# Kernel tuning notes

Measured on AMD Instinct MI355X. Metric: run time of the kernel, lower is better.

Reference implementation:

```python
import jax, jax.numpy as jnp
import numpy as np


def _build_idx():
    # Gather indices replicating the 36 overlapping 3x3 window slices.
    # Board layout: flat index = x*48 + y*6 + f  (8x8 squares, 6 features).
    idx = np.zeros((36, 54), dtype=np.int32)
    for i in range(36):
        x, y = i // 6, i % 6
        c = 0
        for ox in range(3):
            for oy in range(3):
                base = (x + ox) * 48 + (y + oy) * 6
                for f in range(6):
                    idx[i, c] = base + f
                    c += 1
    return jnp.asarray(idx)

IDX = _build_idx()  # [36, 54]
B = 65536


def setup_inputs() -> dict:
    key = jax.random.key(0)
    ks = jax.random.split(key, 13)
    rn = lambda k, shape, s=0.3: jax.random.normal(k, shape, dtype=jnp.float32) * s
    return {
        "inp": jax.random.normal(ks[0], (B, 385), dtype=jnp.float32),
        "W1": rn(ks[1], (16, 54)), "b1": rn(ks[2], (16,)),
        "W2": rn(ks[3], (16, 16)), "b2": rn(ks[4], (16,)),
        "W3": rn(ks[5], (2, 16)),  "b3": rn(ks[6], (2,)),
        "E1": rn(ks[7], (34, 73)), "e1": rn(ks[8], (34,)),
        "E2": rn(ks[9], (34, 34)), "e2": rn(ks[10], (34,)),
        "E3": rn(ks[11], (1, 34)), "e3": rn(ks[12], (1,)),
    }


def reference(inp, W1, b1, W2, b2, W3, b3, E1, e1, E2, e2, E3, e3):
    crelu = lambda x: jnp.clip(x, -1.0, 1.0)
    # One gather replaces 36 * 9 slice/cat ops: [B, 36, 54]
    w = inp[:, IDX]
    # Sight MLP applied to all 36 windows at once (torch Linear: x @ W.T + b)
    h = crelu(jnp.einsum('bws,os->bwo', w, W1) + b1)   # [B, 36, 16]
    h = crelu(jnp.einsum('bwi,oi->bwo', h, W2) + b2)   # [B, 36, 16]
    v = crelu(jnp.einsum('bwi,oi->bwo', h, W3) + b3)   # [B, 36, 2]
    # vision[i*2], vision[i*2+1] interleave == reshape of [36, 2]; append inp[384]
    vision = jnp.concatenate([v.reshape(v.shape[0], 72), inp[:, 384:385]], axis=-1)  # [B, 73]
    h = crelu(vision @ E1.T + e1)
    h = crelu(h @ E2.T + e2)
    return crelu(h @ E3.T + e3)  # [B, 1]
```

## Files before the change

### kernel.cpp

```cpp
#include <hip/hip_runtime.h>
#include <hip/hip_fp16.h>

typedef _Float16 half8v __attribute__((ext_vector_type(8)));
typedef __fp16  pk16x2 __attribute__((ext_vector_type(2)));
typedef float f32x4 __attribute__((ext_vector_type(4)));

#define DEV __device__ __forceinline__
DEV float crelu(float x) { return fminf(fmaxf(x, -1.0f), 1.0f); }

DEV unsigned int pkrtz_u32(float a, float b) {
    pk16x2 p = __builtin_amdgcn_cvt_pkrtz(a, b);
    return __builtin_bit_cast(unsigned int, p);
}

DEV void lgkm0() { asm volatile("s_waitcnt lgkmcnt(0)" ::: "memory"); }
DEV void cfence() { asm volatile("" ::: "memory"); }

__global__ void prep_kernel(const float* __restrict__ W1, const float* __restrict__ W2,
                            const float* __restrict__ W3, const float* __restrict__ E1,
                            const float* __restrict__ E2, const float* __restrict__ e1b,
                            const float* __restrict__ e2b, const float* __restrict__ E3,
                            float* __restrict__ ws) {
    int t = threadIdx.x + blockIdx.x * blockDim.x;
    if (t < 864) {
        int s = t >> 4, o = t & 15;
        ws[t] = W1[o * 54 + s];
    } else if (t < 864 + 256) {
        int u = t - 864; int i = u >> 4, o = u & 15;
        ws[t] = W2[o * 16 + i];
    } else if (t < 1120 + 32) {
        int u = t - 1120; int i = u >> 1, o = u & 1;
        ws[t] = W3[o * 16 + i];
    } else if (t >= 8192 && t < 8192 + 1536) {
        _Float16* fr = (_Float16*)((char*)ws + 19200);
        int u = t - 8192;
        int ks = u >> 9, l = (u >> 3) & 63, j = u & 7;
        int n = l & 15;
        int kg = ks * 32 + ((l >> 4) << 3) + j;
        int ox = kg / 24, rem = kg - ox * 24, cy = rem >> 3, f = rem & 7;
        float v = (kg < 72 && f < 6) ? W1[n * 54 + ox * 18 + cy * 6 + f] : 0.0f;
        fr[u] = (_Float16)v;
    } else if (t >= 10240 && t < 10240 + 512) {
        _Float16* fr = (_Float16*)((char*)ws + 19200) + 1536;
        int u = t - 10240;
        int l = u >> 3, j = u & 7;
        int n = l & 15;
        int k = ((l >> 4) << 3) + j;
        float v = (k < 16) ? W2[n * 16 + k] : 0.0f;
        fr[u] = (_Float16)v;
    } else if (t >= 12288 && t < 12288 + 4608) {
        _Float16* fr = (_Float16*)((char*)ws + 32768);
        int u = t - 12288;
        int ks = u / 1536, rem = u % 1536;
        int nt = rem / 512;
        int l = (rem >> 3) & 63, j = u & 7;
        int k = ks * 32 + ((l >> 4) << 3) + j;
        int o = nt * 16 + (l & 15);
        float v = (k < 73 && o < 34) ? E1[o * 73 + k] : 0.0f;
        fr[u] = (_Float16)v;
    } else if (t >= 18432 && t < 18432 + 3072) {
        _Float16* fr = (_Float16*)((char*)ws + 45056);
        int u = t - 18432;
        int ks = u / 1536, rem = u % 1536;
        int nt = rem / 512;
        int l = (rem >> 3) & 63, j = u & 7;
        int k = ks * 32 + ((l >> 4) << 3) + j;
        int o = nt * 16 + (l & 15);
        float v = (k < 34 && o < 34) ? E2[o * 34 + k] : 0.0f;
        fr[u] = (_Float16)v;
    } else if (t >= 22528 && t < 22528 + 48) {
        int u = t - 22528; ws[6000 + u] = (u < 34) ? e1b[u] : 0.0f;
    } else if (t >= 22592 && t < 22592 + 48) {
        int u = t - 22592; ws[6048 + u] = (u < 34) ? e2b[u] : 0.0f;
    } else if (t >= 22656 && t < 22656 + 48) {
        int u = t - 22656; ws[6096 + u] = (u < 34) ? E3[u] : 0.0f;
    }
}

__global__ __launch_bounds__(256, 3) void win_kernel(
    const float* __restrict__ inp,
    const float* __restrict__ b1, const float* __restrict__ b2,
    const float* __restrict__ b3,
    const float* __restrict__ ws, const _Float16* __restrict__ frag,
    unsigned int* __restrict__ vout)
{
    __shared__ half8v lds[4 * 580];
    const int tid  = threadIdx.x;
    const int wid  = tid >> 6;
    const int lane = tid & 63;
    const int baseP = (blockIdx.x * 4 + wid) * 4;

    half8v* grid = lds + wid * 580;
    half8v* h1   = grid + 288;
    _Float16* h1h = (_Float16*)h1;

    const int r = lane & 15;
    const int g = lane >> 4;

    {
        const uint4 z = {0u, 0u, 0u, 0u};
        #pragma unroll
        for (int i = 0; i < 10; ++i) {
            const int idx = lane + i * 64;
            if (i < 9 || idx < 580)
                *reinterpret_cast<uint4*>(grid + idx) = z;
        }
    }
    cfence();

    {
        const int es = lane >> 4, m = lane & 15;
        const float* __restrict__ src = inp + (size_t)(baseP + es) * 385 + 24 * m;
        #pragma unroll
        for (int c = 0; c < 4; ++c) {
            float f0 = src[c * 6 + 0], f1 = src[c * 6 + 1], f2 = src[c * 6 + 2];
            float f3 = src[c * 6 + 3], f4 = src[c * 6 + 4], f5 = src[c * 6 + 5];
            uint4 q;
            q.x = pkrtz_u32(f0, f1);
            q.y = pkrtz_u32(f2, f3);
            q.z = pkrtz_u32(f4, f5);
            q.w = q.z;
            *reinterpret_cast<uint4*>(grid + es * 72 + 4 * m + c) = q;
        }
    }
    cfence();

    const half8v* __restrict__ fr8 = (const half8v*)frag;
    half8v B1_0 = fr8[0 * 64 + lane];
    half8v B1_1 = fr8[1 * 64 + lane];
    half8v B1_2 = fr8[2 * 64 + lane];
    half8v B2f  = fr8[3 * 64 + lane];

    int off[3];
    #pragma unroll
    for (int ks = 0; ks < 3; ++ks) {
        int c = ks * 4 + g;
        int ox = c / 3, cy = c - 3 * ox;
        off[ks] = ox * 8 + cy;
    }

    const float bias1 = b1[r];
    const float bias2 = b2[r];
    const float* __restrict__ w3t = ws + 1120;
    const float b30 = b3[0], b31 = b3[1];

    int w = r, ebase = 0;
    #pragma unroll
    for (int t = 0; t < 9; ++t) {
        const int x = (w * 43) >> 8;
        const int y = w - x * 6;
        const int cellb = ebase + x * 8 + y;

        half8v a0 = grid[cellb + off[0]];
        half8v a1 = grid[cellb + off[1]];
        half8v a2 = grid[cellb + off[2]];

        f32x4 acc = {bias1, bias1, bias1, bias1};
        acc = __builtin_amdgcn_mfma_f32_16x16x32_f16(a0, B1_0, acc, 0, 0, 0);
        acc = __builtin_amdgcn_mfma_f32_16x16x32_f16(a1, B1_1, acc, 0, 0, 0);
        acc = __builtin_amdgcn_mfma_f32_16x16x32_f16(a2, B1_2, acc, 0, 0, 0);

        #pragma unroll
        for (int q = 0; q < 4; ++q)
            h1h[(t * 16 + g * 4 + q) * 16 + r] = (_Float16)crelu(acc[q]);
        cfence();

        half8v af = h1[(t * 16 + r) * 2 + g];
        f32x4 c2 = {bias2, bias2, bias2, bias2};
        c2 = __builtin_amdgcn_mfma_f32_16x16x32_f16(af, B2f, c2, 0, 0, 0);

        #pragma unroll
        for (int q = 0; q < 4; ++q)
            h1h[(t * 16 + g * 4 + q) * 16 + r] = (_Float16)crelu(c2[q]);

        w += 16;
        if (w >= 36) { w -= 36; ebase += 72; }
    }
    cfence();

    #pragma unroll
    for (int rep = 0; rep < 3; ++rep) {
        const int wg = lane + rep * 64;
        if (rep < 2 || lane < 16) {
            half8v ha = h1[wg * 2 + 0];
            half8v hb = h1[wg * 2 + 1];
            float v0 = b30, v1 = b31;
            #pragma unroll
            for (int i = 0; i < 8; ++i) {
                const float hv = (float)ha[i];
                v0 = fmaf(hv, w3t[i * 2 + 0], v0);
                v1 = fmaf(hv, w3t[i * 2 + 1], v1);
            }
            #pragma unroll
            for (int i = 0; i < 8; ++i) {
                const float hv = (float)hb[i];
                v0 = fmaf(hv, w3t[(8 + i) * 2 + 0], v0);
                v1 = fmaf(hv, w3t[(8 + i) * 2 + 1], v1);
            }
            vout[baseP * 36 + wg] = pkrtz_u32(crelu(v0), crelu(v1));
        }
    }
}

__global__ __launch_bounds__(256) void head3b_kernel(
    const float* __restrict__ inp,
    const float* __restrict__ ws,
    const unsigned int* __restrict__ vbuf,
    const float* __restrict__ e3v,
    float* __restrict__ out)
{
    __shared__ _Float16 hset[4][17 * 48];
    const int tid  = threadIdx.x;
    const int wid  = tid >> 6;
    const int lane = tid & 63;
    const int baseE = (blockIdx.x * 4 + wid) * 16;

    const int r = lane & 15;
    const int g = lane >> 4;
    _Float16* hw = hset[wid];

    {
        const uint4 z = {0u, 0u, 0u, 0u};
        if (lane < 51) {
            *reinterpret_cast<uint4*>(hw + lane * 8) = z;
            *reinterpret_cast<uint4*>(hw + (lane + 51) * 8) = z;
        }
    }
    lgkm0();

    const half8v* __restrict__ e1f8 = (const half8v*)((const char*)ws + 32768);
    const half8v* __restrict__ e2f8 = (const half8v*)((const char*)ws + 45056);

    half8v e1B[3][3], e2B[2][3];
    #pragma unroll
    for (int ks = 0; ks < 3; ++ks)
        #pragma unroll
        for (int nt = 0; nt < 3; ++nt)
            e1B[ks][nt] = e1f8[(ks * 3 + nt) * 64 + lane];
    #pragma unroll
    for (int ks = 0; ks < 2; ++ks)
        #pragma unroll
        for (int nt = 0; nt < 3; ++nt)
            e2B[ks][nt] = e2f8[(ks * 3 + nt) * 64 + lane];

    float biasA[3], bias2A[3], e3w[3];
    #pragma unroll
    for (int nt = 0; nt < 3; ++nt) {
        biasA[nt]  = ws[6000 + nt * 16 + r];
        bias2A[nt] = ws[6048 + nt * 16 + r];
        e3w[nt]    = ws[6096 + nt * 16 + r];
    }

    const uint4* __restrict__ vp4 =
        (const uint4*)(vbuf + (size_t)(baseE + r) * 36);
    const float xl = inp[(size_t)(baseE + r) * 385 + 384];

    f32x4 acc[3] = {{biasA[0], biasA[0], biasA[0], biasA[0]},
                    {biasA[1], biasA[1], biasA[1], biasA[1]},
                    {biasA[2], biasA[2], biasA[2], biasA[2]}};
    #pragma unroll
    for (int ks = 0; ks < 3; ++ks) {
        uint4 aw;
        if (ks < 2) {
            aw = vp4[ks * 4 + g];
        } else {
            if (g == 0)      aw = vp4[8];
            else if (g == 1) { aw.x = pkrtz_u32(xl, 0.0f); aw.y = 0u; aw.z = 0u; aw.w = 0u; }
            else             { aw.x = 0u; aw.y = 0u; aw.z = 0u; aw.w = 0u; }
        }
        const half8v af = __builtin_bit_cast(half8v, aw);
        #pragma unroll
        for (int nt = 0; nt < 3; ++nt)
            acc[nt] = __builtin_amdgcn_mfma_f32_16x16x32_f16(af, e1B[ks][nt],
                                                             acc[nt], 0, 0, 0);
    }

    #pragma unroll
    for (int nt = 0; nt < 3; ++nt)
        #pragma unroll
        for (int q = 0; q < 4; ++q)
            hw[(g * 4 + q) * 48 + nt * 16 + r] = (_Float16)crelu(acc[nt][q]);
    lgkm0();

    f32x4 acc2[3] = {{bias2A[0], bias2A[0], bias2A[0], bias2A[0]},
                     {bias2A[1], bias2A[1], bias2A[1], bias2A[1]},
                     {bias2A[2], bias2A[2], bias2A[2], bias2A[2]}};
    #pragma unroll
    for (int ks = 0; ks < 2; ++ks) {
        const half8v af = *reinterpret_cast<const half8v*>(
            &hw[r * 48 + ks * 32 + g * 8]);
        #pragma unroll
        for (int nt = 0; nt < 3; ++nt)
            acc2[nt] = __builtin_amdgcn_mfma_f32_16x16x32_f16(af, e2B[ks][nt],
                                                              acc2[nt], 0, 0, 0);
    }

    const float e3b = e3v[0];
    float s[4];
    #pragma unroll
    for (int q = 0; q < 4; ++q) {
        float part = crelu(acc2[0][q]) * e3w[0]
                   + crelu(acc2[1][q]) * e3w[1]
                   + crelu(acc2[2][q]) * e3w[2];
        part += __shfl_xor(part, 1);
        part += __shfl_xor(part, 2);
        part += __shfl_xor(part, 4);
        part += __shfl_xor(part, 8);
        s[q] = crelu(part + e3b);
    }
    if (r == 0) {
        float4 o4 = {s[0], s[1], s[2], s[3]};
        *reinterpret_cast<float4*>(out + baseE + g * 4) = o4;
    }
}

extern "C" void kernel_launch(void* const* d_in, const int* in_sizes, int n_in,
                              void* d_out, int out_size, void* d_ws, size_t ws_size,
                              hipStream_t stream) {
    const float* inp = (const float*)d_in[0];
    const float* W1  = (const float*)d_in[1];
    const float* b1  = (const float*)d_in[2];
    const float* W2  = (const float*)d_in[3];
    const float* b2  = (const float*)d_in[4];
    const float* W3  = (const float*)d_in[5];
    const float* b3  = (const float*)d_in[6];
    const float* E1  = (const float*)d_in[7];
    const float* e1  = (const float*)d_in[8];
    const float* E2  = (const float*)d_in[9];
    const float* e2  = (const float*)d_in[10];
    const float* E3  = (const float*)d_in[11];
    const float* e3  = (const float*)d_in[12];
    float* out = (float*)d_out;
    float* ws  = (float*)d_ws;
    const _Float16* frag = (const _Float16*)((const char*)d_ws + 19200);
    unsigned int* vbuf = (unsigned int*)((char*)d_ws + 65536);

    prep_kernel<<<89, 256, 0, stream>>>(W1, W2, W3, E1, E2, e1, e2, E3, ws);

    const int B = 65536;
    win_kernel<<<B / 16, 256, 0, stream>>>(inp, b1, b2, b3, ws, frag, vbuf);
    head3b_kernel<<<B / 64, 256, 0, stream>>>(inp, ws, vbuf, e3, out);
}
```

Baseline: 42.83 us.

## Fuse layer-3 projection into window loop and shrink per-wave LDS buffer

```diff
diff --git a/kernel.cpp b/kernel.cpp
--- a/kernel.cpp
+++ b/kernel.cpp
@@ -2,6 +2,7 @@
 #include <hip/hip_fp16.h>
 
 typedef _Float16 half8v __attribute__((ext_vector_type(8)));
+typedef _Float16 half4v __attribute__((ext_vector_type(4)));
 typedef __fp16  pk16x2 __attribute__((ext_vector_type(2)));
 typedef float f32x4 __attribute__((ext_vector_type(4)));
 
@@ -84,13 +85,13 @@
     const float* __restrict__ ws, const _Float16* __restrict__ frag,
     unsigned int* __restrict__ vout)
 {
-    __shared__ half8v lds[4 * 580];
+    __shared__ half8v lds[4 * 322];
     const int tid  = threadIdx.x;
     const int wid  = tid >> 6;
     const int lane = tid & 63;
     const int baseP = (blockIdx.x * 4 + wid) * 4;
 
-    half8v* grid = lds + wid * 580;
+    half8v* grid = lds + wid * 322;
     half8v* h1   = grid + 288;
     _Float16* h1h = (_Float16*)h1;
 
@@ -100,9 +101,9 @@
     {
         const uint4 z = {0u, 0u, 0u, 0u};
         #pragma unroll
-        for (int i = 0; i < 10; ++i) {
+        for (int i = 0; i < 6; ++i) {
             const int idx = lane + i * 64;
-            if (i < 9 || idx < 580)
+            if (i < 5 || idx < 322)
                 *reinterpret_cast<uint4*>(grid + idx) = z;
         }
     }
@@ -142,6 +143,12 @@
     const float bias1 = b1[r];
     const float bias2 = b2[r];
     const float* __restrict__ w3t = ws + 1120;
+    float w3a[4], w3b[4];
+    #pragma unroll
+    for (int q = 0; q < 4; ++q) {
+        w3a[q] = w3t[(g * 4 + q) * 2 + 0];
+        w3b[q] = w3t[(g * 4 + q) * 2 + 1];
+    }
     const float b30 = b3[0], b31 = b3[1];
 
     int w = r, ebase = 0;
@@ -162,43 +169,42 @@
 
         #pragma unroll
         for (int q = 0; q < 4; ++q)
-            h1h[(t * 16 + g * 4 + q) * 16 + r] = (_Float16)crelu(acc[q]);
+            h1h[(g * 4 + q) * 16 + r] = (_Float16)crelu(acc[q]);
         cfence();
 
-        half8v af = h1[(t * 16 + r) * 2 + g];
+        half8v af = h1[r * 2 + g];
         f32x4 c2 = {bias2, bias2, bias2, bias2};
         c2 = __builtin_amdgcn_mfma_f32_16x16x32_f16(af, B2f, c2, 0, 0, 0);
 
         #pragma unroll
         for (int q = 0; q < 4; ++q)
-            h1h[(t * 16 + g * 4 + q) * 16 + r] = (_Float16)crelu(c2[q]);
+            h1h[(g * 4 + q) * 16 + r] = (_Float16)crelu(c2[q]);
+        cfence();
+
+        {
+            const half4v hq = *reinterpret_cast<const half4v*>(
+                h1h + r * 16 + g * 4);
+            float v0p = 0.0f, v1p = 0.0f;
+            #pragma unroll
+            for (int q = 0; q < 4; ++q) {
+                const float hv = (float)hq[q];
+                v0p = fmaf(hv, w3a[q], v0p);
+                v1p = fmaf(hv, w3b[q], v1p);
+            }
+            v0p += __shfl_xor(v0p, 16);
+            v0p += __shfl_xor(v0p, 32);
+            v1p += __shfl_xor(v1p, 16);
+            v1p += __shfl_xor(v1p, 32);
+            if (g == 0) {
+                const int W = (ebase >> 1) + w;
+                vout[baseP * 36 + W] =
+                    pkrtz_u32(crelu(v0p + b30), crelu(v1p + b31));
+            }
+        }
+        cfence();
 
         w += 16;
         if (w >= 36) { w -= 36; ebase += 72; }
-    }
-    cfence();
-
-    #pragma unroll
-    for (int rep = 0; rep < 3; ++rep) {
-        const int wg = lane + rep * 64;
-        if (rep < 2 || lane < 16) {
-            half8v ha = h1[wg * 2 + 0];
-            half8v hb = h1[wg * 2 + 1];
-            float v0 = b30, v1 = b31;
-            #pragma unroll
-            for (int i = 0; i < 8; ++i) {
-                const float hv = (float)ha[i];
-                v0 = fmaf(hv, w3t[i * 2 + 0], v0);
-                v1 = fmaf(hv, w3t[i * 2 + 1], v1);
-            }
-            #pragma unroll
-            for (int i = 0; i < 8; ++i) {
-                const float hv = (float)hb[i];
-                v0 = fmaf(hv, w3t[(8 + i) * 2 + 0], v0);
-                v1 = fmaf(hv, w3t[(8 + i) * 2 + 1], v1);
-            }
-            vout[baseP * 36 + wg] = pkrtz_u32(crelu(v0), crelu(v1));
-        }
     }
 }
 
```

After: 46.87 us. 1.09x slower.

## Fuse window and head kernels, passing vision through shared memory

Applied to the files above, without the earlier changes.

```diff
diff --git a/kernel.cpp b/kernel.cpp
--- a/kernel.cpp
+++ b/kernel.cpp
@@ -77,22 +77,25 @@
     }
 }
 
-__global__ __launch_bounds__(256, 3) void win_kernel(
+__global__ __launch_bounds__(256, 2) void lila_kernel(
     const float* __restrict__ inp,
     const float* __restrict__ b1, const float* __restrict__ b2,
-    const float* __restrict__ b3,
+    const float* __restrict__ b3, const float* __restrict__ e3v,
     const float* __restrict__ ws, const _Float16* __restrict__ frag,
-    unsigned int* __restrict__ vout)
+    float* __restrict__ out)
 {
     __shared__ half8v lds[4 * 580];
     const int tid  = threadIdx.x;
     const int wid  = tid >> 6;
     const int lane = tid & 63;
-    const int baseP = (blockIdx.x * 4 + wid) * 4;
+    const int baseE = blockIdx.x * 16;
+    const int baseP = baseE + wid * 4;
 
     half8v* grid = lds + wid * 580;
     half8v* h1   = grid + 288;
     _Float16* h1h = (_Float16*)h1;
+    unsigned int* vloc = (unsigned int*)lds;
+    _Float16* hset = (_Float16*)((char*)lds + 9280);
 
     const int r = lane & 15;
     const int g = lane >> 4;
@@ -125,123 +128,101 @@
     }
     cfence();
 
-    const half8v* __restrict__ fr8 = (const half8v*)frag;
-    half8v B1_0 = fr8[0 * 64 + lane];
-    half8v B1_1 = fr8[1 * 64 + lane];
-    half8v B1_2 = fr8[2 * 64 + lane];
-    half8v B2f  = fr8[3 * 64 + lane];
-
-    int off[3];
-    #pragma unroll
-    for (int ks = 0; ks < 3; ++ks) {
-        int c = ks * 4 + g;
-        int ox = c / 3, cy = c - 3 * ox;
-        off[ks] = ox * 8 + cy;
-    }
-
-    const float bias1 = b1[r];
-    const float bias2 = b2[r];
-    const float* __restrict__ w3t = ws + 1120;
-    const float b30 = b3[0], b31 = b3[1];
-
-    int w = r, ebase = 0;
-    #pragma unroll
-    for (int t = 0; t < 9; ++t) {
-        const int x = (w * 43) >> 8;
-        const int y = w - x * 6;
-        const int cellb = ebase + x * 8 + y;
-
-        half8v a0 = grid[cellb + off[0]];
-        half8v a1 = grid[cellb + off[1]];
-        half8v a2 = grid[cellb + off[2]];
-
-        f32x4 acc = {bias1, bias1, bias1, bias1};
-        acc = __builtin_amdgcn_mfma_f32_16x16x32_f16(a0, B1_0, acc, 0, 0, 0);
-        acc = __builtin_amdgcn_mfma_f32_16x16x32_f16(a1, B1_1, acc, 0, 0, 0);
-        acc = __builtin_amdgcn_mfma_f32_16x16x32_f16(a2, B1_2, acc, 0, 0, 0);
-
-        #pragma unroll
-        for (int q = 0; q < 4; ++q)
-            h1h[(t * 16 + g * 4 + q) * 16 + r] = (_Float16)crelu(acc[q]);
-        cfence();
-
-        half8v af = h1[(t * 16 + r) * 2 + g];
-        f32x4 c2 = {bias2, bias2, bias2, bias2};
-        c2 = __builtin_amdgcn_mfma_f32_16x16x32_f16(af, B2f, c2, 0, 0, 0);
-
-        #pragma unroll
-        for (int q = 0; q < 4; ++q)
-            h1h[(t * 16 + g * 4 + q) * 16 + r] = (_Float16)crelu(c2[q]);
-
-        w += 16;
-        if (w >= 36) { w -= 36; ebase += 72; }
-    }
-    cfence();
-
-    #pragma unroll
-    for (int rep = 0; rep < 3; ++rep) {
-        const int wg = lane + rep * 64;
-        if (rep < 2 || lane < 16) {
-            half8v ha = h1[wg * 2 + 0];
-            half8v hb = h1[wg * 2 + 1];
-            float v0 = b30, v1 = b31;
+    {
+        const half8v* __restrict__ fr8 = (const half8v*)frag;
+        half8v B1_0 = fr8[0 * 64 + lane];
+        half8v B1_1 = fr8[1 * 64 + lane];
+        half8v B1_2 = fr8[2 * 64 + lane];
+        half8v B2f  = fr8[3 * 64 + lane];
+
+        int off[3];
+        #pragma unroll
+        for (int ks = 0; ks < 3; ++ks) {
+            int c = ks * 4 + g;
+            int ox = c / 3, cy = c - 3 * ox;
+            off[ks] = ox * 8 + cy;
+        }
+
+        const float bias1 = b1[r];
+        const float bias2 = b2[r];
+
+        int w = r, ebase = 0;
+        #pragma unroll
+        for (int t = 0; t < 9; ++t) {
+            const int x = (w * 43) >> 8;
+            const int y = w - x * 6;
+            const int cellb = ebase + x * 8 + y;
+
+            half8v a0 = grid[cellb + off[0]];
+            half8v a1 = grid[cellb + off[1]];
+            half8v a2 = grid[cellb + off[2]];
+
+            f32x4 acc = {bias1, bias1, bias1, bias1};
+            acc = __builtin_amdgcn_mfma_f32_16x16x32_f16(a0, B1_0, acc, 0, 0, 0);
+            acc = __builtin_amdgcn_mfma_f32_16x16x32_f16(a1, B1_1, acc, 0, 0, 0);
+            acc = __builtin_amdgcn_mfma_f32_16x16x32_f16(a2, B1_2, acc, 0, 0, 0);
+
             #pragma unroll
-            for (int i = 0; i < 8; ++i) {
-                const float hv = (float)ha[i];
-                v0 = fmaf(hv, w3t[i * 2 + 0], v0);
-                v1 = fmaf(hv, w3t[i * 2 + 1], v1);
+            for (int q = 0; q < 4; ++q)
+                h1h[(t * 16 + g * 4 + q) * 16 + r] = (_Float16)crelu(acc[q]);
+            cfence();
+
+            half8v af = h1[(t * 16 + r) * 2 + g];
+            f32x4 c2 = {bias2, bias2, bias2, bias2};
+            c2 = __builtin_amdgcn_mfma_f32_16x16x32_f16(af, B2f, c2, 0, 0, 0);
+
+            #pragma unroll
+            for (int q = 0; q < 4; ++q)
+                h1h[(t * 16 + g * 4 + q) * 16 + r] = (_Float16)crelu(c2[q]);
+
+            w += 16;
+            if (w >= 36) { w -= 36; ebase += 72; }
+        }
+    }
+
+    __syncthreads();
+
+    {
+        const float* __restrict__ w3t = ws + 1120;
+        const float b30 = b3[0], b31 = b3[1];
+        #pragma unroll
+        for (int rep = 0; rep < 3; ++rep) {
+            const int wg = lane + rep * 64;
+            if (rep < 2 || lane < 16) {
+                half8v ha = h1[wg * 2 + 0];
+                half8v hb = h1[wg * 2 + 1];
+                float v0 = b30, v1 = b31;
+                #pragma unroll
+                for (int i = 0; i < 8; ++i) {
+                    const float hv = (float)ha[i];
+                    v0 = fmaf(hv, w3t[i * 2 + 0], v0);
+                    v1 = fmaf(hv, w3t[i * 2 + 1], v1);
+                }
+                #pragma unroll
+                for (int i = 0; i < 8; ++i) {
+                    const float hv = (float)hb[i];
+                    v0 = fmaf(hv, w3t[(8 + i) * 2 + 0], v0);
+                    v1 = fmaf(hv, w3t[(8 + i) * 2 + 1], v1);
+                }
+                vloc[wid * 144 + wg] = pkrtz_u32(crelu(v0), crelu(v1));
             }
-            #pragma unroll
-            for (int i = 0; i < 8; ++i) {
-                const float hv = (float)hb[i];
-                v0 = fmaf(hv, w3t[(8 + i) * 2 + 0], v0);
-                v1 = fmaf(hv, w3t[(8 + i) * 2 + 1], v1);
-            }
-            vout[baseP * 36 + wg] = pkrtz_u32(crelu(v0), crelu(v1));
-        }
-    }
-}
-
-__global__ __launch_bounds__(256) void head3b_kernel(
-    const float* __restrict__ inp,
-    const float* __restrict__ ws,
-    const unsigned int* __restrict__ vbuf,
-    const float* __restrict__ e3v,
-    float* __restrict__ out)
-{
-    __shared__ _Float16 hset[4][17 * 48];
-    const int tid  = threadIdx.x;
-    const int wid  = tid >> 6;
-    const int lane = tid & 63;
-    const int baseE = (blockIdx.x * 4 + wid) * 16;
-
-    const int r = lane & 15;
-    const int g = lane >> 4;
-    _Float16* hw = hset[wid];
+        }
+    }
+
+    __syncthreads();
+    if (wid != 0) return;
 
     {
         const uint4 z = {0u, 0u, 0u, 0u};
         if (lane < 51) {
-            *reinterpret_cast<uint4*>(hw + lane * 8) = z;
-            *reinterpret_cast<uint4*>(hw + (lane + 51) * 8) = z;
+            *reinterpret_cast<uint4*>(hset + lane * 8) = z;
+            *reinterpret_cast<uint4*>(hset + (lane + 51) * 8) = z;
         }
     }
     lgkm0();
 
     const half8v* __restrict__ e1f8 = (const half8v*)((const char*)ws + 32768);
     const half8v* __restrict__ e2f8 = (const half8v*)((const char*)ws + 45056);
-
-    half8v e1B[3][3], e2B[2][3];
-    #pragma unroll
-    for (int ks = 0; ks < 3; ++ks)
-        #pragma unroll
-        for (int nt = 0; nt < 3; ++nt)
-            e1B[ks][nt] = e1f8[(ks * 3 + nt) * 64 + lane];
-    #pragma unroll
-    for (int ks = 0; ks < 2; ++ks)
-        #pragma unroll
-        for (int nt = 0; nt < 3; ++nt)
-            e2B[ks][nt] = e2f8[(ks * 3 + nt) * 64 + lane];
 
     float biasA[3], bias2A[3], e3w[3];
     #pragma unroll
@@ -251,8 +232,7 @@
         e3w[nt]    = ws[6096 + nt * 16 + r];
     }
 
-    const uint4* __restrict__ vp4 =
-        (const uint4*)(vbuf + (size_t)(baseE + r) * 36);
+    const uint4* vp4 = (const uint4*)(vloc + r * 36);
     const float xl = inp[(size_t)(baseE + r) * 385 + 384];
 
     f32x4 acc[3] = {{biasA[0], biasA[0], biasA[0], biasA[0]},
@@ -271,15 +251,15 @@
         const half8v af = __builtin_bit_cast(half8v, aw);
         #pragma unroll
         for (int nt = 0; nt < 3; ++nt)
-            acc[nt] = __builtin_amdgcn_mfma_f32_16x16x32_f16(af, e1B[ks][nt],
-                                                             acc[nt], 0, 0, 0);
+            acc[nt] = __builtin_amdgcn_mfma_f32_16x16x32_f16(
+                af, e1f8[(ks * 3 + nt) * 64 + lane], acc[nt], 0, 0, 0);
     }
 
     #pragma unroll
     for (int nt = 0; nt < 3; ++nt)
         #pragma unroll
         for (int q = 0; q < 4; ++q)
-            hw[(g * 4 + q) * 48 + nt * 16 + r] = (_Float16)crelu(acc[nt][q]);
+            hset[(g * 4 + q) * 48 + nt * 16 + r] = (_Float16)crelu(acc[nt][q]);
     lgkm0();
 
     f32x4 acc2[3] = {{bias2A[0], bias2A[0], bias2A[0], bias2A[0]},
@@ -288,11 +268,11 @@
     #pragma unroll
     for (int ks = 0; ks < 2; ++ks) {
         const half8v af = *reinterpret_cast<const half8v*>(
-            &hw[r * 48 + ks * 32 + g * 8]);
+            &hset[r * 48 + ks * 32 + g * 8]);
         #pragma unroll
         for (int nt = 0; nt < 3; ++nt)
-            acc2[nt] = __builtin_amdgcn_mfma_f32_16x16x32_f16(af, e2B[ks][nt],
-                                                              acc2[nt], 0, 0, 0);
+            acc2[nt] = __builtin_amdgcn_mfma_f32_16x16x32_f16(
+                af, e2f8[(ks * 3 + nt) * 64 + lane], acc2[nt], 0, 0, 0);
     }
 
     const float e3b = e3v[0];
@@ -333,11 +313,9 @@
     float* out = (float*)d_out;
     float* ws  = (float*)d_ws;
     const _Float16* frag = (const _Float16*)((const char*)d_ws + 19200);
-    unsigned int* vbuf = (unsigned int*)((char*)d_ws + 65536);
 
     prep_kernel<<<89, 256, 0, stream>>>(W1, W2, W3, E1, E2, e1, e2, E3, ws);
 
     const int B = 65536;
-    win_kernel<<<B / 16, 256, 0, stream>>>(inp, b1, b2, b3, ws, frag, vbuf);
-    head3b_kernel<<<B / 64, 256, 0, stream>>>(inp, ws, vbuf, e3, out);
+    lila_kernel<<<B / 16, 256, 0, stream>>>(inp, b1, b2, b3, e3, ws, frag, out);
 }
```

New measurement: 42.66 us. No clear change (-0.4%).
